# Kernel optimization log

Measured on AMD Instinct MI355X. Metric: run time of the kernel, lower is better.

## Reference

```python
import jax, jax.numpy as jnp
import numpy as np

N_NODES = 100000
N_EDGES = 600000
D = 128
EPS = 1e-12  # F.normalize default eps


def _l2_normalize(v, axis=1):
    n = jnp.linalg.norm(v, axis=axis, keepdims=True)
    return v / jnp.maximum(n, EPS)


def setup_inputs() -> dict:
    key = jax.random.key(0)
    k1, k2, k3, k4, k5 = jax.random.split(key, 5)
    x = jax.random.normal(k1, (N_NODES, D), dtype=jnp.float32)
    edge_index = jax.random.randint(k2, (2, N_EDGES), 0, N_NODES, dtype=jnp.int64)
    edge_weight = jax.random.uniform(k3, (N_EDGES,), dtype=jnp.float32)
    W = jax.random.normal(k4, (D, 2 * D), dtype=jnp.float32) / np.sqrt(2 * D)
    b = jax.random.normal(k5, (D,), dtype=jnp.float32) * 0.01
    return {"x": x, "edge_index": edge_index, "edge_weight": edge_weight, "W": W, "b": b}


def reference(x, edge_index, edge_weight, W, b):
    src, dst = edge_index[0], edge_index[1]
    # message: x_j * edge_weight; aggregate: scatter-add at destination nodes
    msgs = x[src] * edge_weight[:, None]                       # [E, D]
    grads = jax.ops.segment_sum(msgs, dst, num_segments=N_NODES)  # [N, D]
    norm_grads = _l2_normalize(grads, axis=1)
    out = jnp.concatenate((x, norm_grads), axis=1)             # [N, 2D]
    out = out @ W.T + b                                        # Linear(2D -> D)
    return _l2_normalize(out, axis=1)
```

## Files before the change

### kernel.cpp

```cpp
#include <hip/hip_runtime.h>
#include <stdint.h>

typedef __attribute__((ext_vector_type(8))) short short8;
typedef __attribute__((ext_vector_type(4))) float f32x4;

__device__ __forceinline__ uint32_t f2bf1(float f) {
  union { float f; uint32_t u; } c; c.f = f;
  return (c.u + 0x7FFFu + ((c.u >> 16) & 1u)) >> 16;
}
__device__ __forceinline__ uint32_t pack2bf(float lo, float hi) {
  return f2bf1(lo) | (f2bf1(hi) << 16);
}
__device__ __forceinline__ float bflo(uint32_t u) {
  union { uint32_t u; float f; } c; c.u = u << 16; return c.f;
}
__device__ __forceinline__ float bfhi(uint32_t u) {
  union { uint32_t u; float f; } c; c.u = u & 0xFFFF0000u; return c.f;
}


__global__ void __launch_bounds__(256) prep_kernel(
    const int* __restrict__ dst, uint32_t* __restrict__ deg,
    uint32_t* __restrict__ pos,
    const float* __restrict__ x, uint32_t* __restrict__ xbf,
    const float* __restrict__ W, uint32_t* __restrict__ wf,
    int E, int N, int eB, int xB) {
  int b = blockIdx.x;
  int ti = threadIdx.x;
  if (b < eB) {
    int e8 = (b * 256 + ti) * 8;
    if (e8 + 7 < E) {
      int4 da = *reinterpret_cast<const int4*>(dst + e8);
      int4 db = *reinterpret_cast<const int4*>(dst + e8 + 4);
      uint4 pa, pb;
      pa.x = atomicAdd(&deg[da.x], 1u);
      pa.y = atomicAdd(&deg[da.y], 1u);
      pa.z = atomicAdd(&deg[da.z], 1u);
      pa.w = atomicAdd(&deg[da.w], 1u);
      pb.x = atomicAdd(&deg[db.x], 1u);
      pb.y = atomicAdd(&deg[db.y], 1u);
      pb.z = atomicAdd(&deg[db.z], 1u);
      pb.w = atomicAdd(&deg[db.w], 1u);
      *reinterpret_cast<uint4*>(pos + e8) = pa;
      *reinterpret_cast<uint4*>(pos + e8 + 4) = pb;
    } else {
      for (int e = e8; e < E; ++e) pos[e] = atomicAdd(&deg[dst[e]], 1u);
    }
  } else if (b < eB + xB) {
    int n = (b - eB) * 32 + (ti >> 3);
    int c0 = ti & 7;
    if (n >= N) return;
    const float* xp0 = x + (size_t)n * 128 + c0 * 8;
    const float* xp1 = x + (size_t)n * 128 + (c0 + 8) * 8;
    float4 f0 = reinterpret_cast<const float4*>(xp0)[0];
    float4 f1 = reinterpret_cast<const float4*>(xp0)[1];
    float4 f2 = reinterpret_cast<const float4*>(xp1)[0];
    float4 f3 = reinterpret_cast<const float4*>(xp1)[1];
    uint4 pka, pkb;
    pka.x = pack2bf(f0.x, f0.y); pka.y = pack2bf(f0.z, f0.w);
    pka.z = pack2bf(f1.x, f1.y); pka.w = pack2bf(f1.z, f1.w);
    pkb.x = pack2bf(f2.x, f2.y); pkb.y = pack2bf(f2.z, f2.w);
    pkb.z = pack2bf(f3.x, f3.y); pkb.w = pack2bf(f3.z, f3.w);
    *reinterpret_cast<uint4*>(xbf + (size_t)n * 64 + c0 * 4) = pka;
    *reinterpret_cast<uint4*>(xbf + (size_t)n * 64 + (c0 + 8) * 4) = pkb;
  } else {
    int ch = (b - eB - xB) * 256 + ti;
    if (ch < 4096) {
      int nt = ch >> 9, ks = (ch >> 6) & 7, lane = ch & 63;
      int rw = nt * 16 + (lane & 15);
      const float* wp = W + (size_t)rw * 256 + ks * 32 + (lane >> 4) * 8;
      float4 f0 = reinterpret_cast<const float4*>(wp)[0];
      float4 f1 = reinterpret_cast<const float4*>(wp)[1];
      uint4 pk;
      pk.x = pack2bf(f0.x, f0.y); pk.y = pack2bf(f0.z, f0.w);
      pk.z = pack2bf(f1.x, f1.y); pk.w = pack2bf(f1.z, f1.w);
      reinterpret_cast<uint4*>(wf)[ch] = pk;
    }
  }
}

__global__ void __launch_bounds__(256) scan1_kernel(
    const uint32_t* __restrict__ deg, uint32_t* __restrict__ partial,
    uint32_t* __restrict__ bsum, int N) {
  __shared__ uint32_t sm[256];
  int t = threadIdx.x;
  int base = blockIdx.x * 1024 + t * 4;
  uint32_t d0 = 0, d1 = 0, d2 = 0, d3 = 0;
  if (base + 3 < N) {
    uint4 v = *reinterpret_cast<const uint4*>(deg + base);
    d0 = v.x; d1 = v.y; d2 = v.z; d3 = v.w;
  } else {
    if (base + 0 < N) d0 = deg[base + 0];
    if (base + 1 < N) d1 = deg[base + 1];
    if (base + 2 < N) d2 = deg[base + 2];
    if (base + 3 < N) d3 = deg[base + 3];
  }
  uint32_t s4 = d0 + d1 + d2 + d3;
  sm[t] = s4;
  uint32_t v = s4;
  __syncthreads();
  #pragma unroll
  for (int off = 1; off < 256; off <<= 1) {
    uint32_t u = (t >= off) ? sm[t - off] : 0u;
    __syncthreads();
    v += u;
    sm[t] = v;
    __syncthreads();
  }
  uint32_t ex = v - s4;
  if (base + 0 < N) partial[base + 0] = ex;
  if (base + 1 < N) partial[base + 1] = ex + d0;
  if (base + 2 < N) partial[base + 2] = ex + d0 + d1;
  if (base + 3 < N) partial[base + 3] = ex + d0 + d1 + d2;
  if (t == 255) bsum[blockIdx.x] = v;
}

__global__ void __launch_bounds__(1024) scan2_kernel(
    const uint32_t* __restrict__ bsum, uint32_t* __restrict__ boff, int nb) {
  __shared__ uint32_t sm[1024];
  int t = threadIdx.x;
  uint32_t s = (t < nb) ? bsum[t] : 0u;
  sm[t] = s;
  uint32_t v = s;
  __syncthreads();
  #pragma unroll
  for (int off = 1; off < 1024; off <<= 1) {
    uint32_t u = (t >= off) ? sm[t - off] : 0u;
    __syncthreads();
    v += u;
    sm[t] = v;
    __syncthreads();
  }
  if (t < nb) boff[t] = v - s;
}

__global__ void __launch_bounds__(256) fill_kernel(
    const int* __restrict__ src, const int* __restrict__ dst,
    const float* __restrict__ ew, const uint32_t* __restrict__ partial,
    const uint32_t* __restrict__ boff, const uint32_t* __restrict__ pos,
    uint2* __restrict__ pairs, int E) {
  int e = blockIdx.x * 256 + threadIdx.x;
  if (e < E) {
    int d = dst[e];
    union { float f; uint32_t u; } w; w.f = ew[e];
    pairs[partial[d] + boff[d >> 10] + pos[e]] = make_uint2((uint32_t)src[e], w.u);
  }
}

__global__ void __launch_bounds__(256) gather_kernel(
    const uint2* __restrict__ pairs, const uint32_t* __restrict__ partial,
    const uint32_t* __restrict__ boff, const uint32_t* __restrict__ deg,
    const uint32_t* __restrict__ xbf, uint32_t* __restrict__ ngf, int N) {
  int n = blockIdx.x * 4 + (threadIdx.x >> 6);
  if (n >= N) return;
  int lane = threadIdx.x & 63;
  int half = lane >> 5;
  int sl2 = lane & 31;
  uint32_t base = partial[n] + boff[n >> 10];
  int dn = (int)deg[n];

  uint2 mp = (lane < dn) ? pairs[base + lane] : make_uint2(0u, 0u);

  float a0 = 0.f, a1 = 0.f, a2 = 0.f, a3 = 0.f;
  int dcap = dn < 64 ? dn : 64;
  int iters = (dcap + 1) >> 1;
  int itp = (iters + 3) & ~3;
  for (int i = 0; i < itp; i += 4) {
    int k0 = (i + 0) * 2 + half;
    int k1 = (i + 1) * 2 + half;
    int k2 = (i + 2) * 2 + half;
    int k3 = (i + 3) * 2 + half;
    uint32_t s0 = (uint32_t)__shfl((int)mp.x, k0, 64);
    uint32_t s1 = (uint32_t)__shfl((int)mp.x, k1, 64);
    uint32_t s2 = (uint32_t)__shfl((int)mp.x, k2, 64);
    uint32_t s3 = (uint32_t)__shfl((int)mp.x, k3, 64);
    union { uint32_t u; float f; } w0, w1, w2, w3;
    w0.u = (uint32_t)__shfl((int)mp.y, k0, 64);
    w1.u = (uint32_t)__shfl((int)mp.y, k1, 64);
    w2.u = (uint32_t)__shfl((int)mp.y, k2, 64);
    w3.u = (uint32_t)__shfl((int)mp.y, k3, 64);
    uint2 v0 = reinterpret_cast<const uint2*>(xbf + (size_t)s0 * 64)[sl2];
    uint2 v1 = reinterpret_cast<const uint2*>(xbf + (size_t)s1 * 64)[sl2];
    uint2 v2 = reinterpret_cast<const uint2*>(xbf + (size_t)s2 * 64)[sl2];
    uint2 v3 = reinterpret_cast<const uint2*>(xbf + (size_t)s3 * 64)[sl2];
    a0 += w0.f * bflo(v0.x); a1 += w0.f * bfhi(v0.x);
    a2 += w0.f * bflo(v0.y); a3 += w0.f * bfhi(v0.y);
    a0 += w1.f * bflo(v1.x); a1 += w1.f * bfhi(v1.x);
    a2 += w1.f * bflo(v1.y); a3 += w1.f * bfhi(v1.y);
    a0 += w2.f * bflo(v2.x); a1 += w2.f * bfhi(v2.x);
    a2 += w2.f * bflo(v2.y); a3 += w2.f * bfhi(v2.y);
    a0 += w3.f * bflo(v3.x); a1 += w3.f * bfhi(v3.x);
    a2 += w3.f * bflo(v3.y); a3 += w3.f * bfhi(v3.y);
  }
  for (int k = 64 + half; k < dn; k += 2) {
    uint2 p = pairs[base + k];
    union { uint32_t u; float f; } w; w.u = p.y;
    uint2 v = reinterpret_cast<const uint2*>(xbf + (size_t)p.x * 64)[sl2];
    a0 += w.f * bflo(v.x);
    a1 += w.f * bfhi(v.x);
    a2 += w.f * bflo(v.y);
    a3 += w.f * bfhi(v.y);
  }

  a0 += __shfl_xor(a0, 32, 64);
  a1 += __shfl_xor(a1, 32, 64);
  a2 += __shfl_xor(a2, 32, 64);
  a3 += __shfl_xor(a3, 32, 64);

  float ss = a0 * a0 + a1 * a1 + a2 * a2 + a3 * a3;
  ss += __shfl_xor(ss, 1, 64);
  ss += __shfl_xor(ss, 2, 64);
  ss += __shfl_xor(ss, 4, 64);
  ss += __shfl_xor(ss, 8, 64);
  ss += __shfl_xor(ss, 16, 64);
  float scale = 1.0f / fmaxf(sqrtf(ss), 1e-12f);
  if (half == 0) {
    uint2 o;
    o.x = pack2bf(a0 * scale, a1 * scale);
    o.y = pack2bf(a2 * scale, a3 * scale);
    int t = n >> 4, rr = n & 15;
    uint32_t* dstp = ngf +
        ((size_t)(t * 4 + (sl2 >> 3)) * 64 + ((sl2 & 7) >> 1) * 16 + rr) * 4 +
        (sl2 & 1) * 2;
    *reinterpret_cast<uint2*>(dstp) = o;
  }
}

__global__ void __launch_bounds__(256) gemm_kernel(
    const uint32_t* __restrict__ xbf, const uint32_t* __restrict__ ngf,
    const uint32_t* __restrict__ wf, const float* __restrict__ bias,
    float* __restrict__ out, int N) {
  int wid = threadIdx.x >> 6;
  int lane = threadIdx.x & 63;
  int tile = blockIdx.x * 4 + wid;
  int node0 = tile * 32;
  if (node0 >= N) return;
  int r = lane & 15;
  int kg = lane >> 4;
  int t0 = tile * 2;

  short8 a0[8], a1[8];
  {
    const uint32_t* xr0 = xbf + (size_t)(node0 + r) * 64 + kg * 4;
    const uint32_t* xr1 = xr0 + 16 * 64;
    #pragma unroll
    for (int ks = 0; ks < 4; ++ks) {
      a0[ks] = *reinterpret_cast<const short8*>(xr0 + ks * 16);
      a1[ks] = *reinterpret_cast<const short8*>(xr1 + ks * 16);
    }
    #pragma unroll
    for (int ks = 0; ks < 4; ++ks) {
      a0[4 + ks] = *reinterpret_cast<const short8*>(
          ngf + ((size_t)(t0 * 4 + ks) * 64 + lane) * 4);
      a1[4 + ks] = *reinterpret_cast<const short8*>(
          ngf + ((size_t)((t0 + 1) * 4 + ks) * 64 + lane) * 4);
    }
  }

  f32x4 acc0[8], acc1[8];
  #pragma unroll
  for (int nt = 0; nt < 8; ++nt) {
    acc0[nt] = (f32x4){0.f, 0.f, 0.f, 0.f};
    acc1[nt] = (f32x4){0.f, 0.f, 0.f, 0.f};
  }

  #pragma unroll
  for (int nt = 0; nt < 8; ++nt) {
    #pragma unroll
    for (int ks = 0; ks < 8; ++ks) {
      short8 bfrag = *reinterpret_cast<const short8*>(
          wf + ((size_t)(nt * 8 + ks) * 64 + lane) * 4);
      acc0[nt] = __builtin_amdgcn_mfma_f32_16x16x32_bf16(a0[ks], bfrag, acc0[nt], 0, 0, 0);
      acc1[nt] = __builtin_amdgcn_mfma_f32_16x16x32_bf16(a1[ks], bfrag, acc1[nt], 0, 0, 0);
    }
  }

  float bv[8];
  #pragma unroll
  for (int nt = 0; nt < 8; ++nt) bv[nt] = bias[nt * 16 + r];

  #pragma unroll
  for (int st = 0; st < 2; ++st) {
    f32x4* acc = st ? acc1 : acc0;
    int nodeb = node0 + st * 16;
    #pragma unroll
    for (int reg = 0; reg < 4; ++reg) {
      float ss = 0.f;
      #pragma unroll
      for (int nt = 0; nt < 8; ++nt) {
        float v = acc[nt][reg] + bv[nt];
        acc[nt][reg] = v;
        ss += v * v;
      }
      ss += __shfl_xor(ss, 1, 64);
      ss += __shfl_xor(ss, 2, 64);
      ss += __shfl_xor(ss, 4, 64);
      ss += __shfl_xor(ss, 8, 64);
      float scale = 1.0f / fmaxf(sqrtf(ss), 1e-12f);
      float* orow = out + (size_t)(nodeb + kg * 4 + reg) * 128;
      #pragma unroll
      for (int nt = 0; nt < 8; ++nt)
        orow[nt * 16 + r] = acc[nt][reg] * scale;
    }
  }
}

extern "C" void kernel_launch(void* const* d_in, const int* in_sizes, int n_in,
                              void* d_out, int out_size, void* d_ws, size_t ws_size,
                              hipStream_t stream) {
  const float* x    = (const float*)d_in[0];
  const int*   ei   = (const int*)d_in[1];
  const float* ew   = (const float*)d_in[2];
  const float* W    = (const float*)d_in[3];
  const float* bias = (const float*)d_in[4];
  float* out = (float*)d_out;

  int N = in_sizes[0] / 128;
  int E = in_sizes[1] / 2;
  const int* src = ei;
  const int* dst = ei + E;
  int nb = (N + 1023) / 1024;

  uint32_t* ngf = (uint32_t*)d_ws;
  uint32_t* wf  = ngf + (size_t)N * 64;
  uint32_t* xbf = wf + 16384;

  uint32_t* o       = (uint32_t*)d_out;
  uint32_t* deg     = o;
  uint32_t* partial = o + N;
  uint32_t* bsum    = o + 2 * (size_t)N;
  uint32_t* boff    = o + 2 * (size_t)N + 1024;
  uint2*    pairs   = (uint2*)(o + 2 * (size_t)N + 2048);
  uint32_t* pos     = o + 2 * (size_t)N + 2048 + 2 * (size_t)E;

  int eB = (E + 2047) / 2048;
  int xB = (N + 31) / 32;
  hipMemsetAsync(deg, 0, (size_t)N * sizeof(uint32_t), stream);
  prep_kernel<<<eB + xB + 16, 256, 0, stream>>>(
      dst, deg, pos, x, xbf, W, wf, E, N, eB, xB);
  scan1_kernel<<<nb, 256, 0, stream>>>(deg, partial, bsum, N);
  scan2_kernel<<<1, 1024, 0, stream>>>(bsum, boff, nb);
  fill_kernel<<<(E + 255) / 256, 256, 0, stream>>>(src, dst, ew, partial, boff,
                                                   pos, pairs, E);
  gather_kernel<<<(N + 3) / 4, 256, 0, stream>>>(pairs, partial, boff, deg,
                                                 xbf, ngf, N);
  int ntiles32 = (N + 31) / 32;
  gemm_kernel<<<(ntiles32 + 3) / 4, 256, 0, stream>>>(xbf, ngf, wf, bias, out, N);
}
```

Before: 125.0 us.

## Pad degree counters to separate cache lines and fuse fill with x/W conversion

Each node's degree counter now sits 64 bytes apart (stride 16 uint32) so that atomics on different nodes do not share a cache line. The edge-count atomics move into their own kernel. The x and W bf16 conversion moves out of that kernel and is merged with the CSR fill step, which saves one launch and lets the conversion overlap the scattered pair writes. In exchange, the memset and the strided degree reads in scan and gather touch 16x more memory (6.4MB instead of 400KB), and the scan1 loads are no longer vectorized.

```diff
diff --git a/kernel.cpp b/kernel.cpp
--- a/kernel.cpp
+++ b/kernel.cpp
@@ -19,35 +19,100 @@
 }
 
 
-__global__ void __launch_bounds__(256) prep_kernel(
-    const int* __restrict__ dst, uint32_t* __restrict__ deg,
-    uint32_t* __restrict__ pos,
+__global__ void __launch_bounds__(256) count_kernel(
+    const int* __restrict__ dst, uint32_t* __restrict__ degp,
+    uint32_t* __restrict__ pos, int E) {
+  int e8 = (blockIdx.x * 256 + threadIdx.x) * 8;
+  if (e8 + 7 < E) {
+    int4 da = *reinterpret_cast<const int4*>(dst + e8);
+    int4 db = *reinterpret_cast<const int4*>(dst + e8 + 4);
+    uint4 pa, pb;
+    pa.x = atomicAdd(&degp[(size_t)da.x * 16], 1u);
+    pa.y = atomicAdd(&degp[(size_t)da.y * 16], 1u);
+    pa.z = atomicAdd(&degp[(size_t)da.z * 16], 1u);
+    pa.w = atomicAdd(&degp[(size_t)da.w * 16], 1u);
+    pb.x = atomicAdd(&degp[(size_t)db.x * 16], 1u);
+    pb.y = atomicAdd(&degp[(size_t)db.y * 16], 1u);
+    pb.z = atomicAdd(&degp[(size_t)db.z * 16], 1u);
+    pb.w = atomicAdd(&degp[(size_t)db.w * 16], 1u);
+    *reinterpret_cast<uint4*>(pos + e8) = pa;
+    *reinterpret_cast<uint4*>(pos + e8 + 4) = pb;
+  } else {
+    for (int e = e8; e < E; ++e)
+      pos[e] = atomicAdd(&degp[(size_t)dst[e] * 16], 1u);
+  }
+}
+
+__global__ void __launch_bounds__(256) scan1_kernel(
+    const uint32_t* __restrict__ degp, uint32_t* __restrict__ partial,
+    uint32_t* __restrict__ bsum, int N) {
+  __shared__ uint32_t sm[256];
+  int t = threadIdx.x;
+  int base = blockIdx.x * 1024 + t * 4;
+  uint32_t d0 = 0, d1 = 0, d2 = 0, d3 = 0;
+  if (base + 0 < N) d0 = degp[(size_t)(base + 0) * 16];
+  if (base + 1 < N) d1 = degp[(size_t)(base + 1) * 16];
+  if (base + 2 < N) d2 = degp[(size_t)(base + 2) * 16];
+  if (base + 3 < N) d3 = degp[(size_t)(base + 3) * 16];
+  uint32_t s4 = d0 + d1 + d2 + d3;
+  sm[t] = s4;
+  uint32_t v = s4;
+  __syncthreads();
+  #pragma unroll
+  for (int off = 1; off < 256; off <<= 1) {
+    uint32_t u = (t >= off) ? sm[t - off] : 0u;
+    __syncthreads();
+    v += u;
+    sm[t] = v;
+    __syncthreads();
+  }
+  uint32_t ex = v - s4;
+  if (base + 0 < N) partial[base + 0] = ex;
+  if (base + 1 < N) partial[base + 1] = ex + d0;
+  if (base + 2 < N) partial[base + 2] = ex + d0 + d1;
+  if (base + 3 < N) partial[base + 3] = ex + d0 + d1 + d2;
+  if (t == 255) bsum[blockIdx.x] = v;
+}
+
+__global__ void __launch_bounds__(1024) scan2_kernel(
+    const uint32_t* __restrict__ bsum, uint32_t* __restrict__ boff, int nb) {
+  __shared__ uint32_t sm[1024];
+  int t = threadIdx.x;
+  uint32_t s = (t < nb) ? bsum[t] : 0u;
+  sm[t] = s;
+  uint32_t v = s;
+  __syncthreads();
+  #pragma unroll
+  for (int off = 1; off < 1024; off <<= 1) {
+    uint32_t u = (t >= off) ? sm[t - off] : 0u;
+    __syncthreads();
+    v += u;
+    sm[t] = v;
+    __syncthreads();
+  }
+  if (t < nb) boff[t] = v - s;
+}
+
+__global__ void __launch_bounds__(256) fxw_kernel(
+    const int* __restrict__ src, const int* __restrict__ dst,
+    const float* __restrict__ ew, const uint32_t* __restrict__ partial,
+    const uint32_t* __restrict__ boff, const uint32_t* __restrict__ pos,
+    uint2* __restrict__ pairs,
     const float* __restrict__ x, uint32_t* __restrict__ xbf,
     const float* __restrict__ W, uint32_t* __restrict__ wf,
-    int E, int N, int eB, int xB) {
+    int E, int N, int fB, int xB) {
   int b = blockIdx.x;
   int ti = threadIdx.x;
-  if (b < eB) {
-    int e8 = (b * 256 + ti) * 8;
-    if (e8 + 7 < E) {
-      int4 da = *reinterpret_cast<const int4*>(dst + e8);
-      int4 db = *reinterpret_cast<const int4*>(dst + e8 + 4);
-      uint4 pa, pb;
-      pa.x = atomicAdd(&deg[da.x], 1u);
-      pa.y = atomicAdd(&deg[da.y], 1u);
-      pa.z = atomicAdd(&deg[da.z], 1u);
-      pa.w = atomicAdd(&deg[da.w], 1u);
-      pb.x = atomicAdd(&deg[db.x], 1u);
-      pb.y = atomicAdd(&deg[db.y], 1u);
-      pb.z = atomicAdd(&deg[db.z], 1u);
-      pb.w = atomicAdd(&deg[db.w], 1u);
-      *reinterpret_cast<uint4*>(pos + e8) = pa;
-      *reinterpret_cast<uint4*>(pos + e8 + 4) = pb;
-    } else {
-      for (int e = e8; e < E; ++e) pos[e] = atomicAdd(&deg[dst[e]], 1u);
-    }
-  } else if (b < eB + xB) {
-    int n = (b - eB) * 32 + (ti >> 3);
+  if (b < fB) {
+    int e = b * 256 + ti;
+    if (e < E) {
+      int d = dst[e];
+      union { float f; uint32_t u; } w; w.f = ew[e];
+      pairs[partial[d] + boff[d >> 10] + pos[e]] =
+          make_uint2((uint32_t)src[e], w.u);
+    }
+  } else if (b < fB + xB) {
+    int n = (b - fB) * 32 + (ti >> 3);
     int c0 = ti & 7;
     if (n >= N) return;
     const float* xp0 = x + (size_t)n * 128 + c0 * 8;
@@ -64,7 +129,7 @@
     *reinterpret_cast<uint4*>(xbf + (size_t)n * 64 + c0 * 4) = pka;
     *reinterpret_cast<uint4*>(xbf + (size_t)n * 64 + (c0 + 8) * 4) = pkb;
   } else {
-    int ch = (b - eB - xB) * 256 + ti;
+    int ch = (b - fB - xB) * 256 + ti;
     if (ch < 4096) {
       int nt = ch >> 9, ks = (ch >> 6) & 7, lane = ch & 63;
       int rw = nt * 16 + (lane & 15);
@@ -79,77 +144,9 @@
   }
 }
 
-__global__ void __launch_bounds__(256) scan1_kernel(
-    const uint32_t* __restrict__ deg, uint32_t* __restrict__ partial,
-    uint32_t* __restrict__ bsum, int N) {
-  __shared__ uint32_t sm[256];
-  int t = threadIdx.x;
-  int base = blockIdx.x * 1024 + t * 4;
-  uint32_t d0 = 0, d1 = 0, d2 = 0, d3 = 0;
-  if (base + 3 < N) {
-    uint4 v = *reinterpret_cast<const uint4*>(deg + base);
-    d0 = v.x; d1 = v.y; d2 = v.z; d3 = v.w;
-  } else {
-    if (base + 0 < N) d0 = deg[base + 0];
-    if (base + 1 < N) d1 = deg[base + 1];
-    if (base + 2 < N) d2 = deg[base + 2];
-    if (base + 3 < N) d3 = deg[base + 3];
-  }
-  uint32_t s4 = d0 + d1 + d2 + d3;
-  sm[t] = s4;
-  uint32_t v = s4;
-  __syncthreads();
-  #pragma unroll
-  for (int off = 1; off < 256; off <<= 1) {
-    uint32_t u = (t >= off) ? sm[t - off] : 0u;
-    __syncthreads();
-    v += u;
-    sm[t] = v;
-    __syncthreads();
-  }
-  uint32_t ex = v - s4;
-  if (base + 0 < N) partial[base + 0] = ex;
-  if (base + 1 < N) partial[base + 1] = ex + d0;
-  if (base + 2 < N) partial[base + 2] = ex + d0 + d1;
-  if (base + 3 < N) partial[base + 3] = ex + d0 + d1 + d2;
-  if (t == 255) bsum[blockIdx.x] = v;
-}
-
-__global__ void __launch_bounds__(1024) scan2_kernel(
-    const uint32_t* __restrict__ bsum, uint32_t* __restrict__ boff, int nb) {
-  __shared__ uint32_t sm[1024];
-  int t = threadIdx.x;
-  uint32_t s = (t < nb) ? bsum[t] : 0u;
-  sm[t] = s;
-  uint32_t v = s;
-  __syncthreads();
-  #pragma unroll
-  for (int off = 1; off < 1024; off <<= 1) {
-    uint32_t u = (t >= off) ? sm[t - off] : 0u;
-    __syncthreads();
-    v += u;
-    sm[t] = v;
-    __syncthreads();
-  }
-  if (t < nb) boff[t] = v - s;
-}
-
-__global__ void __launch_bounds__(256) fill_kernel(
-    const int* __restrict__ src, const int* __restrict__ dst,
-    const float* __restrict__ ew, const uint32_t* __restrict__ partial,
-    const uint32_t* __restrict__ boff, const uint32_t* __restrict__ pos,
-    uint2* __restrict__ pairs, int E) {
-  int e = blockIdx.x * 256 + threadIdx.x;
-  if (e < E) {
-    int d = dst[e];
-    union { float f; uint32_t u; } w; w.f = ew[e];
-    pairs[partial[d] + boff[d >> 10] + pos[e]] = make_uint2((uint32_t)src[e], w.u);
-  }
-}
-
 __global__ void __launch_bounds__(256) gather_kernel(
     const uint2* __restrict__ pairs, const uint32_t* __restrict__ partial,
-    const uint32_t* __restrict__ boff, const uint32_t* __restrict__ deg,
+    const uint32_t* __restrict__ boff, const uint32_t* __restrict__ degp,
     const uint32_t* __restrict__ xbf, uint32_t* __restrict__ ngf, int N) {
   int n = blockIdx.x * 4 + (threadIdx.x >> 6);
   if (n >= N) return;
@@ -157,7 +154,7 @@
   int half = lane >> 5;
   int sl2 = lane & 31;
   uint32_t base = partial[n] + boff[n >> 10];
-  int dn = (int)deg[n];
+  int dn = (int)degp[(size_t)n * 16];
 
   uint2 mp = (lane < dn) ? pairs[base + lane] : make_uint2(0u, 0u);
 
@@ -326,23 +323,22 @@
   uint32_t* xbf = wf + 16384;
 
   uint32_t* o       = (uint32_t*)d_out;
-  uint32_t* deg     = o;
-  uint32_t* partial = o + N;
-  uint32_t* bsum    = o + 2 * (size_t)N;
-  uint32_t* boff    = o + 2 * (size_t)N + 1024;
-  uint2*    pairs   = (uint2*)(o + 2 * (size_t)N + 2048);
-  uint32_t* pos     = o + 2 * (size_t)N + 2048 + 2 * (size_t)E;
-
-  int eB = (E + 2047) / 2048;
+  uint32_t* degp    = o;
+  uint32_t* partial = o + (size_t)N * 16;
+  uint32_t* bsum    = partial + N;
+  uint32_t* boff    = bsum + 1024;
+  uint2*    pairs   = (uint2*)(boff + 1024);
+  uint32_t* pos     = (uint32_t*)(pairs + E);
+
+  hipMemsetAsync(degp, 0, (size_t)N * 16 * sizeof(uint32_t), stream);
+  count_kernel<<<(E + 2047) / 2048, 256, 0, stream>>>(dst, degp, pos, E);
+  scan1_kernel<<<nb, 256, 0, stream>>>(degp, partial, bsum, N);
+  scan2_kernel<<<1, 1024, 0, stream>>>(bsum, boff, nb);
+  int fB = (E + 255) / 256;
   int xB = (N + 31) / 32;
-  hipMemsetAsync(deg, 0, (size_t)N * sizeof(uint32_t), stream);
-  prep_kernel<<<eB + xB + 16, 256, 0, stream>>>(
-      dst, deg, pos, x, xbf, W, wf, E, N, eB, xB);
-  scan1_kernel<<<nb, 256, 0, stream>>>(deg, partial, bsum, N);
-  scan2_kernel<<<1, 1024, 0, stream>>>(bsum, boff, nb);
-  fill_kernel<<<(E + 255) / 256, 256, 0, stream>>>(src, dst, ew, partial, boff,
-                                                   pos, pairs, E);
-  gather_kernel<<<(N + 3) / 4, 256, 0, stream>>>(pairs, partial, boff, deg,
+  fxw_kernel<<<fB + xB + 16, 256, 0, stream>>>(
+      src, dst, ew, partial, boff, pos, pairs, x, xbf, W, wf, E, N, fB, xB);
+  gather_kernel<<<(N + 3) / 4, 256, 0, stream>>>(pairs, partial, boff, degp,
                                                  xbf, ngf, N);
   int ntiles32 = (N + 31) / 32;
   gemm_kernel<<<(ntiles32 + 3) / 4, 256, 0, stream>>>(xbf, ngf, wf, bias, out, N);
```

After: 130.1 us. +4.1%, slower.
